# Performance work log

Hardware: AMD Instinct MI355X
Metric: run time of the kernel (lower is better)

## Reference

```python
import jax, jax.numpy as jnp
import numpy as np

B, DZ, H, DY = 4096, 512, 2048, 10
N_STEPS = 64
SCALE = 0.02  # matches param_ulow/uhigh magnitude


def setup_inputs() -> dict:
    key = jax.random.key(0)
    ks = jax.random.split(key, 6)
    x = jax.random.normal(ks[0], (B, DZ), dtype=jnp.float32)
    A = jax.random.normal(ks[1], (DZ, DZ), dtype=jnp.float32) * SCALE
    W1 = jax.random.normal(ks[2], (H, DZ), dtype=jnp.float32) * SCALE
    b1 = jax.random.normal(ks[3], (H,), dtype=jnp.float32) * SCALE
    W2 = jax.random.normal(ks[4], (DY, H), dtype=jnp.float32) * SCALE
    b2 = jax.random.normal(ks[5], (DY,), dtype=jnp.float32) * SCALE
    return {"x": x, "A": A, "W1": W1, "b1": b1, "W2": W2, "b2": b2,
            "n_steps": N_STEPS}


def reference(x, A, W1, b1, W2, b2, n_steps):
    # Z0 = P @ x with P = I  => Z0 = x
    # dz/dt = einsum('ji,bi->bj', A, z) = z @ A.T ; explicit Euler on [0, 1]
    dt = jnp.float32(1.0 / n_steps)

    def euler_step(z, _):
        return z + dt * (z @ A.T), None

    zT, _ = jax.lax.scan(euler_step, x, None, length=n_steps)  # [B, DZ]
    # Q MLP (n_layers=3): Linear -> ReLU -> Linear
    h = jax.nn.relu(zT @ W1.T + b1)  # [B, H]
    y = h @ W2.T + b2                # [B, DY]
    return y
```

## Files before the change

kernel.cpp:

```cpp
#include <hip/hip_runtime.h>
#include <hip/hip_bf16.h>

#define B_SZ 4096
#define DZ   512
#define H_SZ 2048
#define DY   10

#define C2 0.4921875f
#define C3 0.158935546875f
#define C4 0.037872314453125f
#define C5 ((float)(7624512.0/1073741824.0))
#define C6 ((float)(74974368.0/68719476736.0))

typedef __attribute__((ext_vector_type(8))) __bf16 bf16x8;
typedef __attribute__((ext_vector_type(4))) float  f32x4;
typedef __attribute__((ext_vector_type(8))) unsigned short us8;

__device__ inline unsigned short f2bf(float f) {
    unsigned u = __float_as_uint(f);
    u += 0x7fffu + ((u >> 16) & 1u);
    return (unsigned short)(u >> 16);
}
__device__ inline float bf2f(unsigned short s) {
    return __uint_as_float(((unsigned)s) << 16);
}

union SqSmem {
    struct { unsigned short A[64 * 64]; unsigned short B[64 * 64]; } s;
    float epi[64 * 68];
};

#define MFMA_STEP(acc)                                                        \
    {                                                                         \
        _Pragma("unroll")                                                     \
        for (int ks = 0; ks < 2; ++ks) {                                      \
            bf16x8 af[2], bfr[2];                                             \
            _Pragma("unroll")                                                 \
            for (int i = 0; i < 2; ++i) {                                     \
                int ra = wm + i * 16 + l16, ca = (ks * 4 + quad) ^ (ra & 7);  \
                af[i] = *(const bf16x8*)&sm.s.A[ra * 64 + ca * 8];            \
                int rb = wn + i * 16 + l16, cb = (ks * 4 + quad) ^ (rb & 7);  \
                bfr[i] = *(const bf16x8*)&sm.s.B[rb * 64 + cb * 8];           \
            }                                                                 \
            _Pragma("unroll")                                                 \
            for (int i = 0; i < 2; ++i)                                       \
                _Pragma("unroll")                                             \
                for (int j = 0; j < 2; ++j)                                   \
                    acc[i][j] = __builtin_amdgcn_mfma_f32_16x16x32_bf16(      \
                        af[i], bfr[j], acc[i][j], 0, 0, 0);                   \
        }                                                                     \
    }

#define ACC_TO_EPI(acc)                                                       \
    {                                                                         \
        _Pragma("unroll")                                                     \
        for (int i = 0; i < 2; ++i)                                           \
            _Pragma("unroll")                                                 \
            for (int j = 0; j < 2; ++j)                                       \
                _Pragma("unroll")                                             \
                for (int rr = 0; rr < 4; ++rr)                                \
                    sm.epi[(wm + i * 16 + quad * 4 + rr) * 68 +               \
                           wn + j * 16 + l16] = acc[i][j][rr];                \
        __syncthreads();                                                      \
    }

__device__ inline void gemm64_mfma(const unsigned short* __restrict__ Arows,
                                   const unsigned short* __restrict__ Brows,
                                   int m0, int n0, int t, SqSmem& sm) {
    const int lane = t & 63, w = t >> 6, quad = lane >> 4, l16 = lane & 15;
    const int wm = (w & 1) * 32, wn = (w >> 1) * 32;
    f32x4 acc[2][2];
#pragma unroll
    for (int i = 0; i < 2; ++i)
#pragma unroll
        for (int j = 0; j < 2; ++j) acc[i][j] = (f32x4){0.f, 0.f, 0.f, 0.f};
    for (int kt = 0; kt < 8; ++kt) {
#pragma unroll
        for (int c = 0; c < 2; ++c) {
            int idx = c * 256 + t, row = idx >> 3, cc = idx & 7;
            int ccs = cc ^ (row & 7);
            *(us8*)&sm.s.A[row * 64 + ccs * 8] =
                *(const us8*)&Arows[(size_t)(m0 + row) * 512 + kt * 64 + cc * 8];
            *(us8*)&sm.s.B[row * 64 + ccs * 8] =
                *(const us8*)&Brows[(size_t)(n0 + row) * 512 + kt * 64 + cc * 8];
        }
        __syncthreads();
        MFMA_STEP(acc)
        __syncthreads();
    }
    ACC_TO_EPI(acc)
}

__device__ inline void gemm64_f32src(const float* __restrict__ Arows,
                                     const float* __restrict__ Bsrc,
                                     int m0, int n0, int t, SqSmem& sm) {
    const int lane = t & 63, w = t >> 6, quad = lane >> 4, l16 = lane & 15;
    const int wm = (w & 1) * 32, wn = (w >> 1) * 32;
    const int r = t >> 2, cq = t & 3;
    f32x4 acc[2][2];
#pragma unroll
    for (int i = 0; i < 2; ++i)
#pragma unroll
        for (int j = 0; j < 2; ++j) acc[i][j] = (f32x4){0.f, 0.f, 0.f, 0.f};
    for (int kt = 0; kt < 8; ++kt) {
        float va[16];
#pragma unroll
        for (int u = 0; u < 4; ++u) {
            float4 f = *(const float4*)&Arows[(size_t)(m0 + r) * 512 + kt * 64 + cq * 16 + u * 4];
            va[u * 4 + 0] = f.x; va[u * 4 + 1] = f.y;
            va[u * 4 + 2] = f.z; va[u * 4 + 3] = f.w;
        }
#pragma unroll
        for (int j2 = 0; j2 < 2; ++j2) {
            us8 h;
#pragma unroll
            for (int j = 0; j < 8; ++j) h[j] = f2bf(va[j2 * 8 + j]);
            int cc = cq * 2 + j2;
            *(us8*)&sm.s.A[r * 64 + (cc ^ (r & 7)) * 8] = h;
        }
#pragma unroll
        for (int u = 0; u < 4; ++u) {
            float4 f = *(const float4*)&Bsrc[(size_t)(kt * 64 + r) * 512 + n0 + cq * 16 + u * 4];
            float vv[4] = {f.x, f.y, f.z, f.w};
#pragma unroll
            for (int j = 0; j < 4; ++j) {
                int n = cq * 16 + u * 4 + j;
                sm.s.B[n * 64 + ((r >> 3) ^ (n & 7)) * 8 + (r & 7)] = f2bf(vv[j]);
            }
        }
        __syncthreads();
        MFMA_STEP(acc)
        __syncthreads();
    }
    ACC_TO_EPI(acc)
}

__device__ inline void epi_out_bf(unsigned short* __restrict__ dst, int m0,
                                  int n0, int t, SqSmem& sm) {
    const int r = t >> 2, cq = t & 3;
    us8 h0, h1;
#pragma unroll
    for (int j = 0; j < 8; ++j) {
        h0[j] = f2bf(sm.epi[r * 68 + cq * 16 + j]);
        h1[j] = f2bf(sm.epi[r * 68 + cq * 16 + 8 + j]);
    }
    *(us8*)&dst[(size_t)(m0 + r) * 512 + n0 + cq * 16]     = h0;
    *(us8*)&dst[(size_t)(m0 + r) * 512 + n0 + cq * 16 + 8] = h1;
}
__device__ inline void epi_out_bfT(unsigned short* __restrict__ dst, int m0,
                                   int n0, int t, SqSmem& sm) {
    const int cf = t >> 2, rq = t & 3;
    us8 o0, o1;
#pragma unroll
    for (int i = 0; i < 8; ++i) {
        o0[i] = f2bf(sm.epi[(rq * 16 + i) * 68 + cf]);
        o1[i] = f2bf(sm.epi[(rq * 16 + 8 + i) * 68 + cf]);
    }
    *(us8*)&dst[(size_t)(n0 + cf) * 512 + m0 + rq * 16]     = o0;
    *(us8*)&dst[(size_t)(n0 + cf) * 512 + m0 + rq * 16 + 8] = o1;
}

__global__ __launch_bounds__(256) void k_s1(
    const float* __restrict__ A, const float* __restrict__ x,
    const float* __restrict__ W1, const float* __restrict__ b2,
    unsigned short* __restrict__ A2_bf, unsigned short* __restrict__ A2T_bf,
    unsigned short* __restrict__ AT_bf, unsigned short* __restrict__ U1_bf,
    unsigned short* __restrict__ x_bf, float* __restrict__ y) {
    __shared__ SqSmem sm;
    const int b = blockIdx.x, t = threadIdx.x;
    const int gid = b * 256 + t;

    const float4* x4 = (const float4*)x;
#pragma unroll
    for (int i = 0; i < 3; ++i) {
        int id = gid + i * 98304;
        if (id < 262144) {
            float4 v0 = x4[(size_t)id * 2], v1 = x4[(size_t)id * 2 + 1];
            us8 o;
            o[0] = f2bf(v0.x); o[1] = f2bf(v0.y); o[2] = f2bf(v0.z); o[3] = f2bf(v0.w);
            o[4] = f2bf(v1.x); o[5] = f2bf(v1.y); o[6] = f2bf(v1.z); o[7] = f2bf(v1.w);
            *(us8*)&x_bf[(size_t)id * 8] = o;
        }
    }
    if (gid < B_SZ * DY) y[gid] = b2[gid % 10];

    if (b < 64) {
        const int m0 = (b >> 3) * 64, n0 = (b & 7) * 64;
        gemm64_f32src(A, A, m0, n0, t, sm);
        epi_out_bf(A2_bf, m0, n0, t, sm);
        epi_out_bfT(A2T_bf, m0, n0, t, sm);
    } else if (b < 128) {
        const int bb = b - 64, m0 = (bb >> 3) * 64, n0 = (bb & 7) * 64;
        const int r = t >> 2, cq = t & 3;
#pragma unroll
        for (int u = 0; u < 4; ++u) {
            float4 f = *(const float4*)&A[(size_t)(m0 + r) * 512 + n0 + cq * 16 + u * 4];
            sm.epi[r * 68 + cq * 16 + u * 4 + 0] = f.x;
            sm.epi[r * 68 + cq * 16 + u * 4 + 1] = f.y;
            sm.epi[r * 68 + cq * 16 + u * 4 + 2] = f.z;
            sm.epi[r * 68 + cq * 16 + u * 4 + 3] = f.w;
        }
        __syncthreads();
        epi_out_bfT(AT_bf, m0, n0, t, sm);
    } else {
        const int bb = b - 128, m0 = (bb >> 3) * 64, n0 = (bb & 7) * 64;
        gemm64_f32src(W1, A, m0, n0, t, sm);
        epi_out_bf(U1_bf, m0, n0, t, sm);
    }
}

__global__ __launch_bounds__(256) void k_s2(
    const unsigned short* __restrict__ A2_bf,
    const unsigned short* __restrict__ A2T_bf,
    const unsigned short* __restrict__ AT_bf,
    const unsigned short* __restrict__ U1_bf,
    unsigned short* __restrict__ A3T_bf, unsigned short* __restrict__ U2_bf,
    unsigned short* __restrict__ U3_bf) {
    __shared__ SqSmem sm;
    const int b = blockIdx.x, t = threadIdx.x;
    if (b < 64) {
        const int m0 = (b >> 3) * 64, n0 = (b & 7) * 64;
        gemm64_mfma(A2_bf, AT_bf, m0, n0, t, sm);
        epi_out_bfT(A3T_bf, m0, n0, t, sm);
    } else if (b < 320) {
        const int bb = b - 64, m0 = (bb >> 3) * 64, n0 = (bb & 7) * 64;
        gemm64_mfma(U1_bf, AT_bf, m0, n0, t, sm);
        epi_out_bf(U2_bf, m0, n0, t, sm);
    } else {
        const int bb = b - 320, m0 = (bb >> 3) * 64, n0 = (bb & 7) * 64;
        gemm64_mfma(U1_bf, A2T_bf, m0, n0, t, sm);
        epi_out_bf(U3_bf, m0, n0, t, sm);
    }
}

__global__ __launch_bounds__(256) void k_s3(
    const float* __restrict__ W1, const unsigned short* __restrict__ U1_bf,
    const unsigned short* __restrict__ U2_bf,
    const unsigned short* __restrict__ U3_bf,
    const unsigned short* __restrict__ A3T_bf,
    unsigned short* __restrict__ w1f) {
    __shared__ SqSmem sm;
    const int b = blockIdx.x, t = threadIdx.x;
    const int m0 = (b >> 3) * 64, n0 = (b & 7) * 64;
    const int lane = t & 63, w = t >> 6, quad = lane >> 4, l16 = lane & 15;
    const int wm = (w & 1) * 32, wn = (w >> 1) * 32;
    f32x4 acc[2][2];
#pragma unroll
    for (int i = 0; i < 2; ++i)
#pragma unroll
        for (int j = 0; j < 2; ++j) acc[i][j] = (f32x4){0.f, 0.f, 0.f, 0.f};
    for (int kt = 0; kt < 8; ++kt) {
#pragma unroll
        for (int c = 0; c < 2; ++c) {
            int idx = c * 256 + t, row = idx >> 3, cc = idx & 7;
            int ccs = cc ^ (row & 7);
            size_t ga = (size_t)(m0 + row) * 512 + kt * 64 + cc * 8;
            us8 u1 = *(const us8*)&U1_bf[ga];
            us8 u2 = *(const us8*)&U2_bf[ga];
            us8 u3 = *(const us8*)&U3_bf[ga];
            us8 g;
#pragma unroll
            for (int j = 0; j < 8; ++j)
                g[j] = f2bf(C4 * bf2f(u1[j]) + C5 * bf2f(u2[j]) + C6 * bf2f(u3[j]));
            *(us8*)&sm.s.A[row * 64 + ccs * 8] = g;
            *(us8*)&sm.s.B[row * 64 + ccs * 8] =
                *(const us8*)&A3T_bf[(size_t)(n0 + row) * 512 + kt * 64 + cc * 8];
        }
        __syncthreads();
        MFMA_STEP(acc)
        __syncthreads();
    }
    ACC_TO_EPI(acc)
    const int r = t >> 2, cq = t & 3;
    size_t gbase = (size_t)(m0 + r) * 512 + n0 + cq * 16;
    us8 u1a = *(const us8*)&U1_bf[gbase], u1b = *(const us8*)&U1_bf[gbase + 8];
    us8 u2a = *(const us8*)&U2_bf[gbase], u2b = *(const us8*)&U2_bf[gbase + 8];
    us8 u3a = *(const us8*)&U3_bf[gbase], u3b = *(const us8*)&U3_bf[gbase + 8];
    us8 h0, h1;
#pragma unroll
    for (int u = 0; u < 2; ++u) {
        float4 wv = *(const float4*)&W1[gbase + u * 4];
        float4 wv2 = *(const float4*)&W1[gbase + 8 + u * 4];
#pragma unroll
        for (int j = 0; j < 4; ++j) {
            int e = u * 4 + j;
            float wj = (j == 0 ? wv.x : j == 1 ? wv.y : j == 2 ? wv.z : wv.w);
            float wj2 = (j == 0 ? wv2.x : j == 1 ? wv2.y : j == 2 ? wv2.z : wv2.w);
            h0[e] = f2bf(wj + bf2f(u1a[e]) + C2 * bf2f(u2a[e]) +
                         C3 * bf2f(u3a[e]) + sm.epi[r * 68 + cq * 16 + e]);
            h1[e] = f2bf(wj2 + bf2f(u1b[e]) + C2 * bf2f(u2b[e]) +
                         C3 * bf2f(u3b[e]) + sm.epi[r * 68 + cq * 16 + 8 + e]);
        }
    }
    *(us8*)&w1f[gbase]     = h0;
    *(us8*)&w1f[gbase + 8] = h1;
}

union SmemU {
    struct { unsigned short A[64 * 64]; unsigned short B[128 * 64]; } s;
    struct { unsigned short h[64 * 136]; } e;
};

__global__ __launch_bounds__(256) void mlp_kernel(
    const unsigned short* __restrict__ x_bf,
    const unsigned short* __restrict__ w1f,
    const float* __restrict__ b1, const float* __restrict__ W2,
    float* __restrict__ y) {
    __shared__ SmemU sm;
    const int t    = threadIdx.x;
    const int lane = t & 63, w = t >> 6;
    const int quad = lane >> 4, l16 = lane & 15;
    const int wn = w * 32;
    const int m0g = blockIdx.x * 64, n0g = blockIdx.y * 128;

    f32x4 acc[4][2];
#pragma unroll
    for (int i = 0; i < 4; ++i)
#pragma unroll
        for (int j = 0; j < 2; ++j) acc[i][j] = (f32x4){0.f, 0.f, 0.f, 0.f};

    for (int kt = 0; kt < 8; ++kt) {
#pragma unroll
        for (int c = 0; c < 2; ++c) {
            int idx = c * 256 + t, row = idx >> 3, cc = idx & 7;
            int ccs = cc ^ (row & 7);
            *(us8*)&sm.s.A[row * 64 + ccs * 8] =
                *(const us8*)&x_bf[(size_t)(m0g + row) * 512 + kt * 64 + cc * 8];
        }
#pragma unroll
        for (int c = 0; c < 4; ++c) {
            int idx = c * 256 + t, row = idx >> 3, cc = idx & 7;
            int ccs = cc ^ (row & 7);
            *(us8*)&sm.s.B[row * 64 + ccs * 8] =
                *(const us8*)&w1f[(size_t)(n0g + row) * 512 + kt * 64 + cc * 8];
        }
        __syncthreads();
#pragma unroll
        for (int ks = 0; ks < 2; ++ks) {
            bf16x8 af[4], bfr[2];
#pragma unroll
            for (int i = 0; i < 4; ++i) {
                int ra = i * 16 + l16, ca = (ks * 4 + quad) ^ (ra & 7);
                af[i] = *(const bf16x8*)&sm.s.A[ra * 64 + ca * 8];
            }
#pragma unroll
            for (int j = 0; j < 2; ++j) {
                int rb = wn + j * 16 + l16, cb = (ks * 4 + quad) ^ (rb & 7);
                bfr[j] = *(const bf16x8*)&sm.s.B[rb * 64 + cb * 8];
            }
#pragma unroll
            for (int i = 0; i < 4; ++i)
#pragma unroll
                for (int j = 0; j < 2; ++j)
                    acc[i][j] = __builtin_amdgcn_mfma_f32_16x16x32_bf16(
                        af[i], bfr[j], acc[i][j], 0, 0, 0);
        }
        __syncthreads();
    }

    float bias[2];
#pragma unroll
    for (int j = 0; j < 2; ++j) bias[j] = b1[n0g + wn + j * 16 + l16];
#pragma unroll
    for (int i = 0; i < 4; ++i)
#pragma unroll
        for (int j = 0; j < 2; ++j)
#pragma unroll
            for (int r = 0; r < 4; ++r) {
                float h = acc[i][j][r] + bias[j];
                h = h > 0.f ? h : 0.f;
                sm.e.h[(i * 16 + quad * 4 + r) * 136 + wn + j * 16 + l16] = f2bf(h);
            }
    __syncthreads();

    {
        bf16x8 wfrag[4];
#pragma unroll
        for (int kc = 0; kc < 4; ++kc) {
            us8 wb;
            if (l16 < DY) {
                const float* wp = &W2[(size_t)l16 * H_SZ + n0g + kc * 32 + quad * 8];
#pragma unroll
                for (int j = 0; j < 8; ++j) wb[j] = f2bf(wp[j]);
            } else {
#pragma unroll
                for (int j = 0; j < 8; ++j) wb[j] = 0;
            }
            wfrag[kc] = *(bf16x8*)&wb;
        }
        f32x4 ay = (f32x4){0.f, 0.f, 0.f, 0.f};
        const int mrow = w * 16;
#pragma unroll
        for (int kc = 0; kc < 4; ++kc) {
            bf16x8 af = *(const bf16x8*)&sm.e.h[(mrow + l16) * 136 + kc * 32 + quad * 8];
            ay = __builtin_amdgcn_mfma_f32_16x16x32_bf16(af, wfrag[kc], ay, 0, 0, 0);
        }
        if (l16 < DY) {
#pragma unroll
            for (int r = 0; r < 4; ++r)
                atomicAdd(&y[(size_t)(m0g + mrow + quad * 4 + r) * DY + l16],
                          ay[r]);
        }
    }
}

extern "C" void kernel_launch(void* const* d_in, const int* in_sizes, int n_in,
                              void* d_out, int out_size, void* d_ws, size_t ws_size,
                              hipStream_t stream) {
    const float* x  = (const float*)d_in[0];
    const float* A  = (const float*)d_in[1];
    const float* W1 = (const float*)d_in[2];
    const float* b1 = (const float*)d_in[3];
    const float* W2 = (const float*)d_in[4];
    const float* b2 = (const float*)d_in[5];
    float* y = (float*)d_out;

    char* ws = (char*)d_ws;
    const size_t HMB = 512u * 1024, MB = 1u << 20;
    unsigned short* AT_bf  = (unsigned short*)(ws);
    unsigned short* A2_bf  = (unsigned short*)(ws + 1 * HMB);
    unsigned short* A2T_bf = (unsigned short*)(ws + 2 * HMB);
    unsigned short* A3T_bf = (unsigned short*)(ws + 3 * HMB);
    unsigned short* U1_bf  = (unsigned short*)(ws + 2 * MB);
    unsigned short* U2_bf  = (unsigned short*)(ws + 4 * MB);
    unsigned short* U3_bf  = (unsigned short*)(ws + 6 * MB);
    unsigned short* w1f    = (unsigned short*)(ws + 8 * MB);
    unsigned short* x_bf   = (unsigned short*)(ws + 10 * MB);

    k_s1<<<384, 256, 0, stream>>>(A, x, W1, b2, A2_bf, A2T_bf, AT_bf, U1_bf,
                                  x_bf, y);
    k_s2<<<576, 256, 0, stream>>>(A2_bf, A2T_bf, AT_bf, U1_bf, A3T_bf, U2_bf,
                                  U3_bf);
    k_s3<<<256, 256, 0, stream>>>(W1, U1_bf, U2_bf, U3_bf, A3T_bf, w1f);
    mlp_kernel<<<dim3(64, 16), dim3(256), 0, stream>>>(x_bf, w1f, b1, W2, y);
}
```

Measured before the change: 139.8 us.

## Stage GEMM tiles with direct global-to-LDS loads and enlarge MLP tile

Global-to-shared staging of the bf16 GEMM operands now uses the global_load_lds builtin, with the XOR swizzle moved onto the global-address side. This skips the round trip through registers in the square GEMM helper, in k_s3's B operand and in the MLP kernel. The first MLP GEMM tile grows from 64x128 to 128x128, with each wave computing a 64x64 sub-tile (4x4 MFMA accumulators), and the grid is halved to match. This improves operand reuse from LDS per load. The costs are more accumulator registers per thread, a larger shared-memory footprint and fewer blocks in flight.

```diff
diff --git a/kernel.cpp b/kernel.cpp
--- a/kernel.cpp
+++ b/kernel.cpp
@@ -25,10 +25,30 @@
     return __uint_as_float(((unsigned)s) << 16);
 }
 
+__device__ __forceinline__ void gl16(const void* g, void* l) {
+    __builtin_amdgcn_global_load_lds(
+        (const __attribute__((address_space(1))) unsigned int*)(size_t)g,
+        (__attribute__((address_space(3))) unsigned int*)(unsigned)(size_t)l,
+        16, 0, 0);
+}
+
 union SqSmem {
     struct { unsigned short A[64 * 64]; unsigned short B[64 * 64]; } s;
     float epi[64 * 68];
 };
+
+__device__ __forceinline__ void stage64(const unsigned short* __restrict__ src,
+                                        unsigned short* lds, int row_base,
+                                        int kt, int t) {
+    const int w = t >> 6, lane = t & 63;
+#pragma unroll
+    for (int i = 0; i < 2; ++i) {
+        int o = w * 128 + i * 64 + lane;
+        int row = o >> 3, cc = (o & 7) ^ (row & 7);
+        gl16(&src[(size_t)(row_base + row) * 512 + kt * 64 + cc * 8],
+             &lds[(size_t)(w * 128 + i * 64) * 8]);
+    }
+}
 
 #define MFMA_STEP(acc)                                                        \
     {                                                                         \
@@ -75,15 +95,8 @@
 #pragma unroll
         for (int j = 0; j < 2; ++j) acc[i][j] = (f32x4){0.f, 0.f, 0.f, 0.f};
     for (int kt = 0; kt < 8; ++kt) {
-#pragma unroll
-        for (int c = 0; c < 2; ++c) {
-            int idx = c * 256 + t, row = idx >> 3, cc = idx & 7;
-            int ccs = cc ^ (row & 7);
-            *(us8*)&sm.s.A[row * 64 + ccs * 8] =
-                *(const us8*)&Arows[(size_t)(m0 + row) * 512 + kt * 64 + cc * 8];
-            *(us8*)&sm.s.B[row * 64 + ccs * 8] =
-                *(const us8*)&Brows[(size_t)(n0 + row) * 512 + kt * 64 + cc * 8];
-        }
+        stage64(Arows, sm.s.A, m0, kt, t);
+        stage64(Brows, sm.s.B, n0, kt, t);
         __syncthreads();
         MFMA_STEP(acc)
         __syncthreads();
@@ -250,6 +263,7 @@
 #pragma unroll
         for (int j = 0; j < 2; ++j) acc[i][j] = (f32x4){0.f, 0.f, 0.f, 0.f};
     for (int kt = 0; kt < 8; ++kt) {
+        stage64(A3T_bf, sm.s.B, n0, kt, t);
 #pragma unroll
         for (int c = 0; c < 2; ++c) {
             int idx = c * 256 + t, row = idx >> 3, cc = idx & 7;
@@ -263,8 +277,6 @@
             for (int j = 0; j < 8; ++j)
                 g[j] = f2bf(C4 * bf2f(u1[j]) + C5 * bf2f(u2[j]) + C6 * bf2f(u3[j]));
             *(us8*)&sm.s.A[row * 64 + ccs * 8] = g;
-            *(us8*)&sm.s.B[row * 64 + ccs * 8] =
-                *(const us8*)&A3T_bf[(size_t)(n0 + row) * 512 + kt * 64 + cc * 8];
         }
         __syncthreads();
         MFMA_STEP(acc)
@@ -297,8 +309,8 @@
 }
 
 union SmemU {
-    struct { unsigned short A[64 * 64]; unsigned short B[128 * 64]; } s;
-    struct { unsigned short h[64 * 136]; } e;
+    struct { unsigned short A[128 * 64]; unsigned short B[128 * 64]; } s;
+    struct { unsigned short h[128 * 136]; } e;
 };
 
 __global__ __launch_bounds__(256) void mlp_kernel(
@@ -310,66 +322,64 @@
     const int t    = threadIdx.x;
     const int lane = t & 63, w = t >> 6;
     const int quad = lane >> 4, l16 = lane & 15;
-    const int wn = w * 32;
-    const int m0g = blockIdx.x * 64, n0g = blockIdx.y * 128;
-
-    f32x4 acc[4][2];
+    const int wm = (w & 1) * 64, wn = (w >> 1) * 64;
+    const int m0g = blockIdx.x * 128, n0g = blockIdx.y * 128;
+
+    f32x4 acc[4][4];
 #pragma unroll
     for (int i = 0; i < 4; ++i)
 #pragma unroll
-        for (int j = 0; j < 2; ++j) acc[i][j] = (f32x4){0.f, 0.f, 0.f, 0.f};
+        for (int j = 0; j < 4; ++j) acc[i][j] = (f32x4){0.f, 0.f, 0.f, 0.f};
 
     for (int kt = 0; kt < 8; ++kt) {
 #pragma unroll
-        for (int c = 0; c < 2; ++c) {
-            int idx = c * 256 + t, row = idx >> 3, cc = idx & 7;
-            int ccs = cc ^ (row & 7);
-            *(us8*)&sm.s.A[row * 64 + ccs * 8] =
-                *(const us8*)&x_bf[(size_t)(m0g + row) * 512 + kt * 64 + cc * 8];
-        }
-#pragma unroll
-        for (int c = 0; c < 4; ++c) {
-            int idx = c * 256 + t, row = idx >> 3, cc = idx & 7;
-            int ccs = cc ^ (row & 7);
-            *(us8*)&sm.s.B[row * 64 + ccs * 8] =
-                *(const us8*)&w1f[(size_t)(n0g + row) * 512 + kt * 64 + cc * 8];
+        for (int i = 0; i < 4; ++i) {
+            int o = w * 256 + i * 64 + lane;
+            int row = o >> 3, cc = (o & 7) ^ (row & 7);
+            gl16(&x_bf[(size_t)(m0g + row) * 512 + kt * 64 + cc * 8],
+                 &sm.s.A[(size_t)(w * 256 + i * 64) * 8]);
+        }
+#pragma unroll
+        for (int i = 0; i < 4; ++i) {
+            int o = w * 256 + i * 64 + lane;
+            int row = o >> 3, cc = (o & 7) ^ (row & 7);
+            gl16(&w1f[(size_t)(n0g + row) * 512 + kt * 64 + cc * 8],
+                 &sm.s.B[(size_t)(w * 256 + i * 64) * 8]);
         }
         __syncthreads();
 #pragma unroll
         for (int ks = 0; ks < 2; ++ks) {
-            bf16x8 af[4], bfr[2];
+            bf16x8 af[4], bfr[4];
 #pragma unroll
             for (int i = 0; i < 4; ++i) {
-                int ra = i * 16 + l16, ca = (ks * 4 + quad) ^ (ra & 7);
+                int ra = wm + i * 16 + l16, ca = (ks * 4 + quad) ^ (ra & 7);
                 af[i] = *(const bf16x8*)&sm.s.A[ra * 64 + ca * 8];
-            }
-#pragma unroll
-            for (int j = 0; j < 2; ++j) {
-                int rb = wn + j * 16 + l16, cb = (ks * 4 + quad) ^ (rb & 7);
-                bfr[j] = *(const bf16x8*)&sm.s.B[rb * 64 + cb * 8];
+                int rb = wn + i * 16 + l16, cb = (ks * 4 + quad) ^ (rb & 7);
+                bfr[i] = *(const bf16x8*)&sm.s.B[rb * 64 + cb * 8];
             }
 #pragma unroll
             for (int i = 0; i < 4; ++i)
 #pragma unroll
-                for (int j = 0; j < 2; ++j)
+                for (int j = 0; j < 4; ++j)
                     acc[i][j] = __builtin_amdgcn_mfma_f32_16x16x32_bf16(
                         af[i], bfr[j], acc[i][j], 0, 0, 0);
         }
         __syncthreads();
     }
 
-    float bias[2];
-#pragma unroll
-    for (int j = 0; j < 2; ++j) bias[j] = b1[n0g + wn + j * 16 + l16];
+    float bias[4];
+#pragma unroll
+    for (int j = 0; j < 4; ++j) bias[j] = b1[n0g + wn + j * 16 + l16];
 #pragma unroll
     for (int i = 0; i < 4; ++i)
 #pragma unroll
-        for (int j = 0; j < 2; ++j)
+        for (int j = 0; j < 4; ++j)
 #pragma unroll
             for (int r = 0; r < 4; ++r) {
                 float h = acc[i][j][r] + bias[j];
                 h = h > 0.f ? h : 0.f;
-                sm.e.h[(i * 16 + quad * 4 + r) * 136 + wn + j * 16 + l16] = f2bf(h);
+                sm.e.h[(wm + i * 16 + quad * 4 + r) * 136 + wn + j * 16 + l16] =
+                    f2bf(h);
             }
     __syncthreads();
 
@@ -388,18 +398,23 @@
             }
             wfrag[kc] = *(bf16x8*)&wb;
         }
-        f32x4 ay = (f32x4){0.f, 0.f, 0.f, 0.f};
-        const int mrow = w * 16;
-#pragma unroll
-        for (int kc = 0; kc < 4; ++kc) {
-            bf16x8 af = *(const bf16x8*)&sm.e.h[(mrow + l16) * 136 + kc * 32 + quad * 8];
-            ay = __builtin_amdgcn_mfma_f32_16x16x32_bf16(af, wfrag[kc], ay, 0, 0, 0);
-        }
-        if (l16 < DY) {
-#pragma unroll
-            for (int r = 0; r < 4; ++r)
-                atomicAdd(&y[(size_t)(m0g + mrow + quad * 4 + r) * DY + l16],
-                          ay[r]);
+#pragma unroll
+        for (int hh = 0; hh < 2; ++hh) {
+            const int mrow = w * 32 + hh * 16;
+            f32x4 ay = (f32x4){0.f, 0.f, 0.f, 0.f};
+#pragma unroll
+            for (int kc = 0; kc < 4; ++kc) {
+                bf16x8 af = *(const bf16x8*)&sm.e.h[(mrow + l16) * 136 +
+                                                    kc * 32 + quad * 8];
+                ay = __builtin_amdgcn_mfma_f32_16x16x32_bf16(af, wfrag[kc], ay,
+                                                             0, 0, 0);
+            }
+            if (l16 < DY) {
+#pragma unroll
+                for (int r = 0; r < 4; ++r)
+                    atomicAdd(&y[(size_t)(m0g + mrow + quad * 4 + r) * DY + l16],
+                              ay[r]);
+            }
         }
     }
 }
@@ -432,5 +447,5 @@
     k_s2<<<576, 256, 0, stream>>>(A2_bf, A2T_bf, AT_bf, U1_bf, A3T_bf, U2_bf,
                                   U3_bf);
     k_s3<<<256, 256, 0, stream>>>(W1, U1_bf, U2_bf, U3_bf, A3T_bf, w1f);
-    mlp_kernel<<<dim3(64, 16), dim3(256), 0, stream>>>(x_bf, w1f, b1, W2, y);
-}
+    mlp_kernel<<<dim3(32, 16), dim3(256), 0, stream>>>(x_bf, w1f, b1, W2, y);
+}
```

Measured after the change: 135.6 us. -3.0%, faster.
